# Kernel optimization log

Hardware: AMD Instinct MI355X
Metric: run time of the kernel (lower is better)

The kernel has to match this reference:

```python
import jax, jax.numpy as jnp
import numpy as np

NUM_HEADS = 16
ROPE_BASE = 10000.0


def _rope(x):
    """Standard rotary embedding. x: (B, H, T, Dh), positions 0..T-1."""
    T, Dh = x.shape[-2], x.shape[-1]
    half = Dh // 2
    inv_freq = 1.0 / (ROPE_BASE ** (jnp.arange(half, dtype=jnp.float32) / half))
    ang = jnp.arange(T, dtype=jnp.float32)[:, None] * inv_freq[None, :]  # (T, half)
    cos, sin = jnp.cos(ang), jnp.sin(ang)
    x1, x2 = x[..., :half], x[..., half:]
    return jnp.concatenate([x1 * cos - x2 * sin, x1 * sin + x2 * cos], axis=-1)


def setup_inputs() -> dict:
    key = jax.random.key(0)
    ks = jax.random.split(key, 5)
    B, N, D = 8, 1025, 1024
    s = 1.0 / np.sqrt(D)
    return {
        "x": jax.random.normal(ks[0], (B, N, D), jnp.float32),
        "wq": jax.random.normal(ks[1], (D, D), jnp.float32) * s,
        "wk": jax.random.normal(ks[2], (D, D), jnp.float32) * s,
        "wv": jax.random.normal(ks[3], (D, D), jnp.float32) * s,
        "q_bias": jnp.zeros((D,), jnp.float32),
        "v_bias": jnp.zeros((D,), jnp.float32),
        "w_out": jax.random.normal(ks[4], (D, D), jnp.float32) * s,
        "b_out": jnp.zeros((D,), jnp.float32),
    }


def reference(x, wq, wk, wv, q_bias, v_bias, w_out, b_out):
    B, N, D = x.shape
    H = NUM_HEADS
    Dh = D // H
    scale = Dh ** -0.5

    q = x @ wq + q_bias           # (B, N, D)
    k = x @ wk
    v = x @ wv + v_bias

    def split_heads(t):  # (B, N, D) -> (B, H, N, Dh)
        return t.reshape(B, N, H, Dh).transpose(0, 2, 1, 3)

    q, k, v = split_heads(q), split_heads(k), split_heads(v)

    # RoPE on all tokens except the first (CLS)
    q = jnp.concatenate([q[:, :, :1, :], _rope(q[:, :, 1:, :])], axis=2)
    k = jnp.concatenate([k[:, :, :1, :], _rope(k[:, :, 1:, :])], axis=2)

    attn = jnp.einsum('bhqd,bhkd->bhqk', q * scale, k)
    attn = jax.nn.softmax(attn, axis=-1)
    out = jnp.einsum('bhqk,bhkd->bhqd', attn, v)  # (B, H, N, Dh)
    out = out.transpose(0, 2, 1, 3).reshape(B, N, D)
    return out @ w_out + b_out
```

## Files before the change

kernel.cpp:

```cpp
#include <hip/hip_runtime.h>

typedef unsigned short u16;
typedef __attribute__((ext_vector_type(8))) short  short8;
typedef __attribute__((ext_vector_type(8))) __bf16 bf16x8;
typedef __attribute__((ext_vector_type(4))) float  f32x4;

#define DEV __device__ __forceinline__

#define BATCH 8
#define SEQ   1025
#define DMODEL 1024
#define NHEAD 16
#define DH    64
#define MROWS (BATCH*SEQ)
#define VPAD  1152
#define KROWS 1088

DEV float bf2f(u16 u) { union { unsigned int i; float f; } v; v.i = ((unsigned int)u) << 16; return v.f; }
DEV u16 f2bf(float f) {
  union { float f; unsigned int i; } v; v.f = f;
  unsigned int x = v.i;
  return (u16)((x + 0x7fffu + ((x >> 16) & 1u)) >> 16);
}

DEV f32x4 mfma16(bf16x8 a, bf16x8 b, f32x4 c) {
  return __builtin_amdgcn_mfma_f32_16x16x32_bf16(a, b, c, 0, 0, 0);
}

DEV void gload_lds16(const void* g, void* s) {
  __builtin_amdgcn_global_load_lds(
      (const __attribute__((address_space(1))) void*)g,
      (__attribute__((address_space(3))) void*)s, 16, 0, 0);
}

DEV float exp2_fast(float x) { float r; asm("v_exp_f32 %0, %1" : "=v"(r) : "v"(x)); return r; }
DEV unsigned cvt_pk_bf16(float lo, float hi) {
  unsigned r;
  asm("v_cvt_pk_bf16_f32 %0, %1, %2" : "=v"(r) : "v"(lo), "v"(hi));
  return r;
}


__global__ void cast_x_kernel(const float* __restrict__ in, u16* __restrict__ out, int n8) {
  int i = blockIdx.x * blockDim.x + threadIdx.x;
  if (i >= n8) return;
  const float4* p = (const float4*)in + (size_t)i * 2;
  float4 a = p[0], b = p[1];
  short8 o;
  o[0] = (short)f2bf(a.x); o[1] = (short)f2bf(a.y); o[2] = (short)f2bf(a.z); o[3] = (short)f2bf(a.w);
  o[4] = (short)f2bf(b.x); o[5] = (short)f2bf(b.y); o[6] = (short)f2bf(b.z); o[7] = (short)f2bf(b.w);
  *(short8*)(out + (size_t)i * 8) = o;
}

__global__ void wt_transpose(const float* __restrict__ wq, const float* __restrict__ wk,
                             const float* __restrict__ wv, const float* __restrict__ wo,
                             u16* __restrict__ wtqkv, u16* __restrict__ wtout) {
  __shared__ float tile[64][65];
  int z = blockIdx.z;
  const float* src = (z == 0) ? wq : (z == 1) ? wk : (z == 2) ? wv : wo;
  int k0 = blockIdx.x * 64, n0 = blockIdx.y * 64;
  int c = threadIdx.x & 63, rq = threadIdx.x >> 6;
#pragma unroll
  for (int p = 0; p < 16; ++p) {
    int r = p * 4 + rq;
    tile[r][c] = src[(size_t)(k0 + r) * 1024 + n0 + c];
  }
  __syncthreads();
  u16* dst = (z < 3) ? (wtqkv + (size_t)z * 1024 * 1024) : wtout;
#pragma unroll
  for (int p = 0; p < 16; ++p) {
    int r = p * 4 + rq;
    dst[(size_t)(n0 + r) * 1024 + k0 + c] = f2bf(tile[c][r]);
  }
}

__global__ void rope_table_kernel(float* __restrict__ cost, float* __restrict__ sint) {
  int i = blockIdx.x * blockDim.x + threadIdx.x;
  if (i >= 1024 * 32) return;
  int pos = i >> 5, d = i & 31;
  float inv = powf(10000.0f, -(float)d / 32.0f);
  float ang = (float)pos * inv;
  cost[i] = cosf(ang);
  sint[i] = sinf(ang);
}

template <int F32OUT>
__global__ __launch_bounds__(256) void gemm128(const u16* __restrict__ A,
    const u16* __restrict__ Bw, void* __restrict__ Cout,
    const float* __restrict__ bias, int Mrows, int ldC) {
  __shared__ char smem[32768];
  const int t = threadIdx.x;
  const int wid = t >> 6, lane = t & 63;
  const int l4 = lane >> 4, l15 = lane & 15;
  const int wr = wid >> 1, wc = wid & 1;
  const long rowA0 = (long)blockIdx.x * 128;
  const long rowB0 = (long)blockIdx.y * 128;

  f32x4 acc[4][4];
#pragma unroll
  for (int m = 0; m < 4; ++m)
#pragma unroll
    for (int n = 0; n < 4; ++n) { f32x4 z = {0.f,0.f,0.f,0.f}; acc[m][n] = z; }

  const int srow = t >> 3;
  const int scol = (t & 7) * 8;

  for (int k0 = 0; k0 < 1024; k0 += 64) {
    __syncthreads();
#pragma unroll
    for (int i = 0; i < 4; ++i) {
      const u16* ga = A  + (rowA0 + i * 32 + srow) * 1024 + k0 + scol;
      gload_lds16(ga, smem + i * 4096 + wid * 1024);
      const u16* gb = Bw + (rowB0 + i * 32 + srow) * 1024 + k0 + scol;
      gload_lds16(gb, smem + 16384 + i * 4096 + wid * 1024);
    }
    __syncthreads();

    bf16x8 af[4][2], bfr[4][2];
#pragma unroll
    for (int m = 0; m < 4; ++m)
#pragma unroll
      for (int kk = 0; kk < 2; ++kk)
        af[m][kk] = *(const bf16x8*)(smem + (wr * 64 + m * 16 + l15) * 128 + kk * 64 + l4 * 16);
#pragma unroll
    for (int n = 0; n < 4; ++n)
#pragma unroll
      for (int kk = 0; kk < 2; ++kk)
        bfr[n][kk] = *(const bf16x8*)(smem + 16384 + (wc * 64 + n * 16 + l15) * 128 + kk * 64 + l4 * 16);

#pragma unroll
    for (int m = 0; m < 4; ++m)
#pragma unroll
      for (int n = 0; n < 4; ++n)
#pragma unroll
        for (int kk = 0; kk < 2; ++kk)
          acc[m][n] = mfma16(af[m][kk], bfr[n][kk], acc[m][n]);
  }

#pragma unroll
  for (int m = 0; m < 4; ++m)
#pragma unroll
    for (int rg = 0; rg < 4; ++rg) {
      long row = rowA0 + wr * 64 + m * 16 + l4 * 4 + rg;
      if (row >= Mrows) continue;
#pragma unroll
      for (int n = 0; n < 4; ++n) {
        long col = rowB0 + wc * 64 + n * 16 + l15;
        float val = acc[m][n][rg];
        if (F32OUT) ((float*)Cout)[row * ldC + col] = val + bias[col];
        else        ((u16*) Cout)[row * ldC + col] = f2bf(val);
      }
    }
}

#define QSCALE (0.125f * 1.44269504088896341f)
__global__ void rope_qk(const u16* __restrict__ cq, const float* __restrict__ qb,
                        const float* __restrict__ cost, const float* __restrict__ sint,
                        u16* __restrict__ Qh, u16* __restrict__ Kh) {
  int idx = blockIdx.x * 256 + threadIdx.x;
  if (idx >= MROWS * NHEAD) return;
  int h = idx & 15, row = idx >> 4;
  int b = row / SEQ, n = row - b * SEQ;
  const u16* src = cq + (size_t)row * 3072 + h * 64;
  size_t dq = ((size_t)(b * 16 + h) * SEQ   + n) * 64;
  size_t dk = ((size_t)(b * 16 + h) * KROWS + n) * 64;
  bool dorope = (n > 0);
  const float* ct = cost + (size_t)(n - 1) * 32;
  const float* st = sint + (size_t)(n - 1) * 32;
#pragma unroll
  for (int i = 0; i < 4; ++i) {
    short8 qlo = *(const short8*)(src + i * 8);
    short8 qhi = *(const short8*)(src + 32 + i * 8);
    short8 klo = *(const short8*)(src + 1024 + i * 8);
    short8 khi = *(const short8*)(src + 1024 + 32 + i * 8);
    short8 oqlo, oqhi, oklo, okhi;
#pragma unroll
    for (int j = 0; j < 8; ++j) {
      int d = i * 8 + j;
      float q1 = bf2f((u16)qlo[j]) + qb[h * 64 + d];
      float q2 = bf2f((u16)qhi[j]) + qb[h * 64 + 32 + d];
      float k1 = bf2f((u16)klo[j]);
      float k2 = bf2f((u16)khi[j]);
      float c = dorope ? ct[d] : 1.0f;
      float s = dorope ? st[d] : 0.0f;
      oqlo[j] = (short)f2bf((q1 * c - q2 * s) * QSCALE);
      oqhi[j] = (short)f2bf((q1 * s + q2 * c) * QSCALE);
      oklo[j] = (short)f2bf(k1 * c - k2 * s);
      okhi[j] = (short)f2bf(k1 * s + k2 * c);
    }
    *(short8*)(Qh + dq + i * 8)      = oqlo;
    *(short8*)(Qh + dq + 32 + i * 8) = oqhi;
    *(short8*)(Kh + dk + i * 8)      = oklo;
    *(short8*)(Kh + dk + 32 + i * 8) = okhi;
  }
}

__global__ void v_transpose(const u16* __restrict__ cq, const float* __restrict__ vb,
                            u16* __restrict__ VTh) {
  __shared__ float tile[64][65];
  int bh = blockIdx.y, b = bh >> 4, h = bh & 15;
  int n0 = blockIdx.x * 64;
  int c = threadIdx.x & 63, rq = threadIdx.x >> 6;
#pragma unroll
  for (int p = 0; p < 16; ++p) {
    int r = p * 4 + rq;
    int n = n0 + r;
    float v = 0.f;
    if (n < SEQ) v = bf2f(cq[(size_t)(b * SEQ + n) * 3072 + 2048 + h * 64 + c]) + vb[h * 64 + c];
    tile[r][c] = v;
  }
  __syncthreads();
#pragma unroll
  for (int p = 0; p < 16; ++p) {
    int d = p * 4 + rq;
    VTh[((size_t)bh * 64 + d) * VPAD + n0 + c] = f2bf(tile[c][d]);
  }
}

DEV void stage_rows(const u16* __restrict__ g, size_t strideElems, char* lbase,
                    int wid, int lane) {
#pragma unroll
  for (int s = 0; s < 2; ++s) {
    int off = s * 4096 + wid * 1024 + lane * 16;
    int r = off >> 7, cs = (off >> 4) & 7;
    const u16* src = g + (size_t)r * strideElems + ((cs ^ (r & 7)) << 3);
    gload_lds16(src, lbase + s * 4096 + wid * 1024);
  }
}

__global__ __launch_bounds__(256, 4) void attn128(const u16* __restrict__ Qh,
    const u16* __restrict__ Kh, const u16* __restrict__ VTh,
    u16* __restrict__ xattn) {
  __shared__ char lds[32768];
  const int wg = blockIdx.x;
  const int x = (wg & 7) * 144 + (wg >> 3);
  const int qt = x % 9, bh = x / 9;
  const int b = bh >> 4, h = bh & 15;
  const int t = threadIdx.x, w = t >> 6, lane = t & 63;
  const int l4 = lane >> 4, l15 = lane & 15;
  const u16* Qb = Qh + (size_t)bh * (SEQ * 64);
  const u16* Kb = Kh + (size_t)bh * (KROWS * 64);
  const u16* Vb = VTh + (size_t)bh * (64 * VPAD);
  const int q0 = qt * 128 + w * 32;
  const int srcb = l15 + ((l4 & 1) << 5);
  const bool hi4 = (l4 >> 1) != 0;

  bf16x8 aq[2][2];
#pragma unroll
  for (int m = 0; m < 2; ++m) {
    int qr = q0 + m * 16 + l15; if (qr > SEQ - 1) qr = SEQ - 1;
    aq[m][0] = *(const bf16x8*)(Qb + (size_t)qr * 64 + l4 * 8);
    aq[m][1] = *(const bf16x8*)(Qb + (size_t)qr * 64 + 32 + l4 * 8);
  }
  bf16x8 ones;
  { union { unsigned u[4]; bf16x8 v; } ou;
    ou.u[0] = ou.u[1] = ou.u[2] = ou.u[3] = 0x3F803F80u; ones = ou.v; }

  f32x4 o[2][4], osum[2];
  float mrow[2];
#pragma unroll
  for (int m = 0; m < 2; ++m) {
#pragma unroll
    for (int n = 0; n < 4; ++n) { f32x4 z = {0.f,0.f,0.f,0.f}; o[m][n] = z; }
    f32x4 z = {0.f,0.f,0.f,0.f}; osum[m] = z;
    mrow[m] = -1e30f;
  }

  stage_rows(Kb, 64, lds, w, lane);
  stage_rows(Vb, VPAD, lds + 16384, w, lane);
  asm volatile("s_waitcnt vmcnt(0)" ::: "memory");
  __syncthreads();

  int cur = 0;
  for (int kt = 0; kt < 17; ++kt) {
    const int kb = kt * 64;
    if (kt < 16) {
      stage_rows(Kb + (size_t)(kb + 64) * 64, 64, lds + (cur ^ 1) * 8192, w, lane);
      stage_rows(Vb + (kb + 64), VPAD, lds + 16384 + (cur ^ 1) * 8192, w, lane);
    }
    const char* Kl = lds + cur * 8192;
    const char* Vl = lds + 16384 + cur * 8192;

    f32x4 s[2][4];
#pragma unroll
    for (int tt = 0; tt < 4; ++tt) {
      const int kr = tt * 16 + l15;
      const char* kp = Kl + kr * 128;
      bf16x8 bk0 = *(const bf16x8*)(kp + ((l4       ^ (kr & 7)) << 4));
      bf16x8 bk1 = *(const bf16x8*)(kp + (((4 + l4) ^ (kr & 7)) << 4));
#pragma unroll
      for (int m = 0; m < 2; ++m) {
        f32x4 z = {0.f,0.f,0.f,0.f};
        z = mfma16(bk0, aq[m][0], z);
        z = mfma16(bk1, aq[m][1], z);
        s[m][tt] = z;
      }
    }

    if (kt == 16) {
#pragma unroll
      for (int m = 0; m < 2; ++m) {
        s[m][0][0] = (l4 == 0) ? s[m][0][0] : -1e30f;
        s[m][0][1] = -1e30f; s[m][0][2] = -1e30f; s[m][0][3] = -1e30f;
#pragma unroll
        for (int tt = 1; tt < 4; ++tt) {
          s[m][tt][0] = -1e30f; s[m][tt][1] = -1e30f; s[m][tt][2] = -1e30f; s[m][tt][3] = -1e30f;
        }
      }
    }

    float tmax[2];
#pragma unroll
    for (int m = 0; m < 2; ++m) {
      float a0 = fmaxf(fmaxf(s[m][0][0], s[m][0][1]), fmaxf(s[m][0][2], s[m][0][3]));
      float a1 = fmaxf(fmaxf(s[m][1][0], s[m][1][1]), fmaxf(s[m][1][2], s[m][1][3]));
      float a2 = fmaxf(fmaxf(s[m][2][0], s[m][2][1]), fmaxf(s[m][2][2], s[m][2][3]));
      float a3 = fmaxf(fmaxf(s[m][3][0], s[m][3][1]), fmaxf(s[m][3][2], s[m][3][3]));
      float tm = fmaxf(fmaxf(a0, a1), fmaxf(a2, a3));
      tm = fmaxf(tm, __shfl_xor(tm, 16));
      tm = fmaxf(tm, __shfl_xor(tm, 32));
      tmax[m] = tm;
    }

    int needR = (tmax[0] > mrow[0] + 8.0f) || (tmax[1] > mrow[1] + 8.0f);
    if (__any(needR)) {
#pragma unroll
      for (int m = 0; m < 2; ++m) {
        float mnew = fmaxf(mrow[m], tmax[m]);
        float alpha = exp2_fast(mrow[m] - mnew);
        mrow[m] = mnew;
        float al[4];
#pragma unroll
        for (int rg = 0; rg < 4; ++rg) al[rg] = __shfl(alpha, l4 * 4 + rg);
#pragma unroll
        for (int n = 0; n < 4; ++n)
#pragma unroll
          for (int rg = 0; rg < 4; ++rg) o[m][n][rg] *= al[rg];
#pragma unroll
        for (int rg = 0; rg < 4; ++rg) osum[m][rg] *= al[rg];
      }
    }

    unsigned pk[2][4][2];
#pragma unroll
    for (int m = 0; m < 2; ++m)
#pragma unroll
      for (int tt = 0; tt < 4; ++tt) {
        float p0 = exp2_fast(s[m][tt][0] - mrow[m]);
        float p1 = exp2_fast(s[m][tt][1] - mrow[m]);
        float p2 = exp2_fast(s[m][tt][2] - mrow[m]);
        float p3 = exp2_fast(s[m][tt][3] - mrow[m]);
        pk[m][tt][0] = cvt_pk_bf16(p0, p1);
        pk[m][tt][1] = cvt_pk_bf16(p2, p3);
      }

#pragma unroll
    for (int kk = 0; kk < 2; ++kk) {
      bf16x8 pa[2];
#pragma unroll
      for (int m = 0; m < 2; ++m) {
        union { unsigned u[4]; bf16x8 v; } pu;
#pragma unroll
        for (int bb = 0; bb < 2; ++bb)
#pragma unroll
          for (int pr = 0; pr < 2; ++pr) {
            unsigned t0 = (unsigned)__shfl((int)pk[m][2 * kk][pr],     srcb + bb * 16);
            unsigned t1 = (unsigned)__shfl((int)pk[m][2 * kk + 1][pr], srcb + bb * 16);
            pu.u[bb * 2 + pr] = hi4 ? t1 : t0;
          }
        pa[m] = pu.v;
      }
#pragma unroll
      for (int n = 0; n < 4; ++n) {
        const int vr = n * 16 + l15;
        bf16x8 bv = *(const bf16x8*)(Vl + vr * 128 + (((kk * 4 + l4) ^ (vr & 7)) << 4));
#pragma unroll
        for (int m = 0; m < 2; ++m)
          o[m][n] = mfma16(pa[m], bv, o[m][n]);
      }
#pragma unroll
      for (int m = 0; m < 2; ++m)
        osum[m] = mfma16(pa[m], ones, osum[m]);
    }

    asm volatile("s_waitcnt vmcnt(0)" ::: "memory");
    __syncthreads();
    cur ^= 1;
  }

#pragma unroll
  for (int m = 0; m < 2; ++m)
#pragma unroll
    for (int n = 0; n < 4; ++n)
#pragma unroll
      for (int rg = 0; rg < 4; ++rg) {
        int qrow = q0 + m * 16 + l4 * 4 + rg;
        if (qrow < SEQ)
          xattn[(size_t)(b * SEQ + qrow) * 1024 + h * 64 + n * 16 + l15] =
              f2bf(o[m][n][rg] / osum[m][rg]);
      }
}


extern "C" void kernel_launch(void* const* d_in, const int* in_sizes, int n_in,
                              void* d_out, int out_size, void* d_ws, size_t ws_size,
                              hipStream_t stream) {
  const float* x      = (const float*)d_in[0];
  const float* wq     = (const float*)d_in[1];
  const float* wk     = (const float*)d_in[2];
  const float* wv     = (const float*)d_in[3];
  const float* q_bias = (const float*)d_in[4];
  const float* v_bias = (const float*)d_in[5];
  const float* w_out  = (const float*)d_in[6];
  const float* b_out  = (const float*)d_in[7];

  char* ws = (char*)d_ws;
  size_t off = 0;
  auto alc = [&](size_t bytes) { size_t r = off; off += (bytes + 255) & ~(size_t)255; return r; };

  u16*  x_bf  = (u16*)(ws + alc((size_t)MROWS * 1024 * 2));
  u16*  wtqkv = (u16*)(ws + alc((size_t)3072 * 1024 * 2));
  u16*  wtout = (u16*)(ws + alc((size_t)1024 * 1024 * 2));
  u16*  xattn = (u16*)(ws + alc((size_t)MROWS * 1024 * 2));
  u16*  cqkv  = (u16*)(ws + alc((size_t)MROWS * 3072 * 2));
  u16*  Qhp   = (u16*)(ws + alc((size_t)128 * SEQ * 64 * 2));
  u16*  Khp   = (u16*)(ws + alc((size_t)128 * KROWS * 64 * 2));
  u16*  VThp  = (u16*)(ws + alc((size_t)128 * 64 * VPAD * 2));
  float* cost = (float*)(ws + alc((size_t)1024 * 32 * 4));
  float* sint = (float*)(ws + alc((size_t)1024 * 32 * 4));
  (void)ws_size; (void)in_sizes; (void)n_in; (void)out_size;

  cast_x_kernel<<<4100, 256, 0, stream>>>(x, x_bf, MROWS * 1024 / 8);
  wt_transpose<<<dim3(16, 16, 4), 256, 0, stream>>>(wq, wk, wv, w_out, wtqkv, wtout);
  rope_table_kernel<<<128, 256, 0, stream>>>(cost, sint);
  gemm128<0><<<dim3(65, 24), 256, 0, stream>>>(x_bf, wtqkv, (void*)cqkv, nullptr, MROWS, 3072);
  rope_qk<<<513, 256, 0, stream>>>(cqkv, q_bias, cost, sint, Qhp, Khp);
  v_transpose<<<dim3(18, 128), 256, 0, stream>>>(cqkv, v_bias, VThp);
  attn128<<<dim3(1152), 256, 0, stream>>>(Qhp, Khp, VThp, xattn);
  gemm128<1><<<dim3(65, 8), 256, 0, stream>>>(xattn, wtout, d_out, b_out, MROWS, 1024);
}
```

Baseline: 294.7 us.

## Fuse RoPE, bias and V transpose into QKV GEMM epilogue; remap tiles for L2

The QKV projection GEMM now applies the q bias, RoPE and Q scaling directly in its epilogue. It also writes Q/K in head-major layout and transposes V through LDS into the padded VT buffer. This removes the intermediate cqkv buffer and two separate kernels, along with their global-memory round trips and launches. Both GEMMs switch to a 1-D grid with a grouped, XCD-aware tile mapping to improve L2 reuse. The trade-off is scattered 2-byte epilogue stores instead of vectorized writes, plus extra epilogue work in the GEMM.

```diff
diff --git a/kernel.cpp b/kernel.cpp
--- a/kernel.cpp
+++ b/kernel.cpp
@@ -38,6 +38,12 @@
   unsigned r;
   asm("v_cvt_pk_bf16_f32 %0, %1, %2" : "=v"(r) : "v"(lo), "v"(hi));
   return r;
+}
+
+DEV void map_tiles(int f, int MT, int NT, int& mt, int& nt) {
+  int body = (MT & ~7) * NT;
+  if (f >= body) { int r = f - body; mt = (MT & ~7) + r / NT; nt = r % NT; }
+  else { int sr = f / (8 * NT); int rem = f - sr * 8 * NT; nt = rem >> 3; mt = sr * 8 + (rem & 7); }
 }
 
 
@@ -84,17 +90,21 @@
   sint[i] = sinf(ang);
 }
 
-template <int F32OUT>
-__global__ __launch_bounds__(256) void gemm128(const u16* __restrict__ A,
-    const u16* __restrict__ Bw, void* __restrict__ Cout,
-    const float* __restrict__ bias, int Mrows, int ldC) {
+#define QSCALE (0.125f * 1.44269504088896341f)
+
+__global__ __launch_bounds__(256) void gemm_qkv(const u16* __restrict__ A,
+    const u16* __restrict__ Bw, const float* __restrict__ qb, const float* __restrict__ vb,
+    const float* __restrict__ ct, const float* __restrict__ st,
+    u16* __restrict__ Qh, u16* __restrict__ Kh, u16* __restrict__ VTh) {
   __shared__ char smem[32768];
+  int mt, nt;
+  { int wg = blockIdx.x; int f = (wg & 7) * 195 + (wg >> 3); map_tiles(f, 65, 24, mt, nt); }
   const int t = threadIdx.x;
   const int wid = t >> 6, lane = t & 63;
   const int l4 = lane >> 4, l15 = lane & 15;
   const int wr = wid >> 1, wc = wid & 1;
-  const long rowA0 = (long)blockIdx.x * 128;
-  const long rowB0 = (long)blockIdx.y * 128;
+  const long rowA0 = (long)mt * 128;
+  const long rowB0 = (long)nt * 128;
 
   f32x4 acc[4][4];
 #pragma unroll
@@ -137,84 +147,139 @@
           acc[m][n] = mfma16(af[m][kk], bfr[n][kk], acc[m][n]);
   }
 
+  const int sel = nt >> 3;
+  const int h = (nt & 7) * 2 + wc;
+
+  if (sel < 2) {
+#pragma unroll
+    for (int m = 0; m < 4; ++m)
+#pragma unroll
+      for (int rg = 0; rg < 4; ++rg) {
+        long row = rowA0 + wr * 64 + m * 16 + l4 * 4 + rg;
+        if (row >= MROWS) continue;
+        int b = (int)(row / SEQ), nl = (int)(row - (long)b * SEQ);
+        bool dorope = nl > 0;
+        const float* ctp = ct + (size_t)(nl - 1) * 32;
+        const float* stp = st + (size_t)(nl - 1) * 32;
+#pragma unroll
+        for (int n = 0; n < 2; ++n) {
+          int d = n * 16 + l15;
+          float c = dorope ? ctp[d] : 1.0f;
+          float s_ = dorope ? stp[d] : 0.0f;
+          float v1 = acc[m][n][rg], v2 = acc[m][n + 2][rg];
+          if (sel == 0) { v1 += qb[h * 64 + d]; v2 += qb[h * 64 + 32 + d]; }
+          float o1 = v1 * c - v2 * s_;
+          float o2 = v1 * s_ + v2 * c;
+          if (sel == 0) {
+            size_t base = ((size_t)(b * 16 + h) * SEQ + nl) * 64 + d;
+            Qh[base]      = f2bf(o1 * QSCALE);
+            Qh[base + 32] = f2bf(o2 * QSCALE);
+          } else {
+            size_t base = ((size_t)(b * 16 + h) * KROWS + nl) * 64 + d;
+            Kh[base]      = f2bf(o1);
+            Kh[base + 32] = f2bf(o2);
+          }
+        }
+      }
+  } else {
+    __syncthreads();
+#pragma unroll
+    for (int m = 0; m < 4; ++m)
+#pragma unroll
+      for (int n = 0; n < 4; ++n) {
+        int co = wc * 64 + n * 16 + l15;
+        int d = n * 16 + l15;
+        float bv = vb[h * 64 + d];
+#pragma unroll
+        for (int rg = 0; rg < 4; ++rg) {
+          int ro = wr * 64 + m * 16 + l4 * 4 + rg;
+          *(u16*)(smem + co * 256 + ((ro * 2) ^ ((co & 7) << 4))) = f2bf(acc[m][n][rg] + bv);
+        }
+      }
+    __syncthreads();
+    const int c = t & 127, half = t >> 7;
+    const int hh = (nt & 7) * 2 + (c >> 6);
+    const int d = c & 63;
+#pragma unroll
+    for (int j = 0; j < 8; ++j) {
+      int t0 = half * 64 + j * 8;
+      short8 v8 = *(const short8*)(smem + c * 256 + ((t0 * 2) ^ ((c & 7) << 4)));
+#pragma unroll
+      for (int e = 0; e < 8; ++e) {
+        long r = rowA0 + t0 + e;
+        if (r >= MROWS) continue;
+        int b = (int)(r / SEQ), nl = (int)(r - (long)b * SEQ);
+        VTh[((size_t)(b * 16 + hh) * 64 + d) * VPAD + nl] = (u16)v8[e];
+      }
+    }
+  }
+}
+
+__global__ __launch_bounds__(256) void gemm_out(const u16* __restrict__ A,
+    const u16* __restrict__ Bw, float* __restrict__ Cout, const float* __restrict__ bias) {
+  __shared__ char smem[32768];
+  int mt, nt;
+  { int wg = blockIdx.x; int f = (wg & 7) * 65 + (wg >> 3); map_tiles(f, 65, 8, mt, nt); }
+  const int t = threadIdx.x;
+  const int wid = t >> 6, lane = t & 63;
+  const int l4 = lane >> 4, l15 = lane & 15;
+  const int wr = wid >> 1, wc = wid & 1;
+  const long rowA0 = (long)mt * 128;
+  const long rowB0 = (long)nt * 128;
+
+  f32x4 acc[4][4];
+#pragma unroll
+  for (int m = 0; m < 4; ++m)
+#pragma unroll
+    for (int n = 0; n < 4; ++n) { f32x4 z = {0.f,0.f,0.f,0.f}; acc[m][n] = z; }
+
+  const int srow = t >> 3;
+  const int scol = (t & 7) * 8;
+
+  for (int k0 = 0; k0 < 1024; k0 += 64) {
+    __syncthreads();
+#pragma unroll
+    for (int i = 0; i < 4; ++i) {
+      const u16* ga = A  + (rowA0 + i * 32 + srow) * 1024 + k0 + scol;
+      gload_lds16(ga, smem + i * 4096 + wid * 1024);
+      const u16* gb = Bw + (rowB0 + i * 32 + srow) * 1024 + k0 + scol;
+      gload_lds16(gb, smem + 16384 + i * 4096 + wid * 1024);
+    }
+    __syncthreads();
+
+    bf16x8 af[4][2], bfr[4][2];
+#pragma unroll
+    for (int m = 0; m < 4; ++m)
+#pragma unroll
+      for (int kk = 0; kk < 2; ++kk)
+        af[m][kk] = *(const bf16x8*)(smem + (wr * 64 + m * 16 + l15) * 128 + kk * 64 + l4 * 16);
+#pragma unroll
+    for (int n = 0; n < 4; ++n)
+#pragma unroll
+      for (int kk = 0; kk < 2; ++kk)
+        bfr[n][kk] = *(const bf16x8*)(smem + 16384 + (wc * 64 + n * 16 + l15) * 128 + kk * 64 + l4 * 16);
+
+#pragma unroll
+    for (int m = 0; m < 4; ++m)
+#pragma unroll
+      for (int n = 0; n < 4; ++n)
+#pragma unroll
+        for (int kk = 0; kk < 2; ++kk)
+          acc[m][n] = mfma16(af[m][kk], bfr[n][kk], acc[m][n]);
+  }
+
 #pragma unroll
   for (int m = 0; m < 4; ++m)
 #pragma unroll
     for (int rg = 0; rg < 4; ++rg) {
       long row = rowA0 + wr * 64 + m * 16 + l4 * 4 + rg;
-      if (row >= Mrows) continue;
+      if (row >= MROWS) continue;
 #pragma unroll
       for (int n = 0; n < 4; ++n) {
         long col = rowB0 + wc * 64 + n * 16 + l15;
-        float val = acc[m][n][rg];
-        if (F32OUT) ((float*)Cout)[row * ldC + col] = val + bias[col];
-        else        ((u16*) Cout)[row * ldC + col] = f2bf(val);
-      }
-    }
-}
-
-#define QSCALE (0.125f * 1.44269504088896341f)
-__global__ void rope_qk(const u16* __restrict__ cq, const float* __restrict__ qb,
-                        const float* __restrict__ cost, const float* __restrict__ sint,
-                        u16* __restrict__ Qh, u16* __restrict__ Kh) {
-  int idx = blockIdx.x * 256 + threadIdx.x;
-  if (idx >= MROWS * NHEAD) return;
-  int h = idx & 15, row = idx >> 4;
-  int b = row / SEQ, n = row - b * SEQ;
-  const u16* src = cq + (size_t)row * 3072 + h * 64;
-  size_t dq = ((size_t)(b * 16 + h) * SEQ   + n) * 64;
-  size_t dk = ((size_t)(b * 16 + h) * KROWS + n) * 64;
-  bool dorope = (n > 0);
-  const float* ct = cost + (size_t)(n - 1) * 32;
-  const float* st = sint + (size_t)(n - 1) * 32;
-#pragma unroll
-  for (int i = 0; i < 4; ++i) {
-    short8 qlo = *(const short8*)(src + i * 8);
-    short8 qhi = *(const short8*)(src + 32 + i * 8);
-    short8 klo = *(const short8*)(src + 1024 + i * 8);
-    short8 khi = *(const short8*)(src + 1024 + 32 + i * 8);
-    short8 oqlo, oqhi, oklo, okhi;
-#pragma unroll
-    for (int j = 0; j < 8; ++j) {
-      int d = i * 8 + j;
-      float q1 = bf2f((u16)qlo[j]) + qb[h * 64 + d];
-      float q2 = bf2f((u16)qhi[j]) + qb[h * 64 + 32 + d];
-      float k1 = bf2f((u16)klo[j]);
-      float k2 = bf2f((u16)khi[j]);
-      float c = dorope ? ct[d] : 1.0f;
-      float s = dorope ? st[d] : 0.0f;
-      oqlo[j] = (short)f2bf((q1 * c - q2 * s) * QSCALE);
-      oqhi[j] = (short)f2bf((q1 * s + q2 * c) * QSCALE);
-      oklo[j] = (short)f2bf(k1 * c - k2 * s);
-      okhi[j] = (short)f2bf(k1 * s + k2 * c);
-    }
-    *(short8*)(Qh + dq + i * 8)      = oqlo;
-    *(short8*)(Qh + dq + 32 + i * 8) = oqhi;
-    *(short8*)(Kh + dk + i * 8)      = oklo;
-    *(short8*)(Kh + dk + 32 + i * 8) = okhi;
-  }
-}
-
-__global__ void v_transpose(const u16* __restrict__ cq, const float* __restrict__ vb,
-                            u16* __restrict__ VTh) {
-  __shared__ float tile[64][65];
-  int bh = blockIdx.y, b = bh >> 4, h = bh & 15;
-  int n0 = blockIdx.x * 64;
-  int c = threadIdx.x & 63, rq = threadIdx.x >> 6;
-#pragma unroll
-  for (int p = 0; p < 16; ++p) {
-    int r = p * 4 + rq;
-    int n = n0 + r;
-    float v = 0.f;
-    if (n < SEQ) v = bf2f(cq[(size_t)(b * SEQ + n) * 3072 + 2048 + h * 64 + c]) + vb[h * 64 + c];
-    tile[r][c] = v;
-  }
-  __syncthreads();
-#pragma unroll
-  for (int p = 0; p < 16; ++p) {
-    int d = p * 4 + rq;
-    VTh[((size_t)bh * 64 + d) * VPAD + n0 + c] = f2bf(tile[c][d]);
-  }
+        Cout[row * 1024 + col] = acc[m][n][rg] + bias[col];
+      }
+    }
 }
 
 DEV void stage_rows(const u16* __restrict__ g, size_t strideElems, char* lbase,
@@ -422,7 +487,6 @@
   u16*  wtqkv = (u16*)(ws + alc((size_t)3072 * 1024 * 2));
   u16*  wtout = (u16*)(ws + alc((size_t)1024 * 1024 * 2));
   u16*  xattn = (u16*)(ws + alc((size_t)MROWS * 1024 * 2));
-  u16*  cqkv  = (u16*)(ws + alc((size_t)MROWS * 3072 * 2));
   u16*  Qhp   = (u16*)(ws + alc((size_t)128 * SEQ * 64 * 2));
   u16*  Khp   = (u16*)(ws + alc((size_t)128 * KROWS * 64 * 2));
   u16*  VThp  = (u16*)(ws + alc((size_t)128 * 64 * VPAD * 2));
@@ -433,9 +497,8 @@
   cast_x_kernel<<<4100, 256, 0, stream>>>(x, x_bf, MROWS * 1024 / 8);
   wt_transpose<<<dim3(16, 16, 4), 256, 0, stream>>>(wq, wk, wv, w_out, wtqkv, wtout);
   rope_table_kernel<<<128, 256, 0, stream>>>(cost, sint);
-  gemm128<0><<<dim3(65, 24), 256, 0, stream>>>(x_bf, wtqkv, (void*)cqkv, nullptr, MROWS, 3072);
-  rope_qk<<<513, 256, 0, stream>>>(cqkv, q_bias, cost, sint, Qhp, Khp);
-  v_transpose<<<dim3(18, 128), 256, 0, stream>>>(cqkv, v_bias, VThp);
+  gemm_qkv<<<dim3(1560), 256, 0, stream>>>(x_bf, wtqkv, q_bias, v_bias, cost, sint,
+                                           Qhp, Khp, VThp);
   attn128<<<dim3(1152), 256, 0, stream>>>(Qhp, Khp, VThp, xattn);
-  gemm128<1><<<dim3(65, 8), 256, 0, stream>>>(xattn, wtout, d_out, b_out, MROWS, 1024);
-}
+  gemm_out<<<dim3(520), 256, 0, stream>>>(xattn, wtout, (float*)d_out, b_out);
+}
```

Result: slower. 305.6 us (+3.7%).

## Replace QKV GEMM with 256x256 double-buffered swizzled LDS kernel and XCD-aware tile mapping

Applied to the files above, without the earlier changes.

The QKV projection now uses a 512-thread kernel with 256x256 output tiles. It double-buffers LDS, prefetching the next K slice while computing the current one. The LDS layout is XOR-swizzled to avoid bank conflicts, and MFMA issue priority is raised. Block indices are remapped so each XCD works on neighbouring tiles for L2 reuse, and the output GEMM gets a similar XCD-grouped tile mapping. The aim is higher arithmetic intensity and hidden load latency. In exchange the kernel uses 128KB of LDS and many accumulator registers, and the last M tile reads past the valid rows into padded workspace.

```diff
diff --git a/kernel.cpp b/kernel.cpp
--- a/kernel.cpp
+++ b/kernel.cpp
@@ -84,17 +84,123 @@
   sint[i] = sinf(ang);
 }
 
-template <int F32OUT>
-__global__ __launch_bounds__(256) void gemm128(const u16* __restrict__ A,
-    const u16* __restrict__ Bw, void* __restrict__ Cout,
-    const float* __restrict__ bias, int Mrows, int ldC) {
+#define QSCALE (0.125f * 1.44269504088896341f)
+
+DEV void stage_issue(const u16* __restrict__ gtile, char* dst, int wid, int lane, int s) {
+  int tt = wid * 64 + lane;
+  int row = s * 64 + (tt >> 3);
+  int cs = (((tt & 7) ^ (row & 7)) << 3);
+  gload_lds16(gtile + (size_t)row * 1024 + cs, dst + s * 8192 + wid * 1024);
+}
+
+__global__ __launch_bounds__(512, 2) void gemm256(const u16* __restrict__ A,
+    const u16* __restrict__ Bw, u16* __restrict__ Cout) {
+  __shared__ char lds[131072];
+  int mt, nt;
+  {
+    int orig = blockIdx.x;
+    int xcd = orig & 7;
+    int f = (xcd < 4 ? xcd * 50 : 200 + (xcd - 4) * 49) + (orig >> 3);
+    if (f < 384) { int sr = f / 48, rem = f % 48; nt = rem >> 2; mt = sr * 4 + (rem & 3); }
+    else { mt = 32; nt = f - 384; }
+  }
+  const int t = threadIdx.x;
+  const int wid = t >> 6, lane = t & 63;
+  const int l4 = lane >> 4, l15 = lane & 15;
+  const int wrow = wid >> 2, wcol = wid & 3;
+  const long rowA0 = (long)mt * 256;
+  const long rowB0 = (long)nt * 256;
+
+  f32x4 acc[8][4];
+#pragma unroll
+  for (int m = 0; m < 8; ++m)
+#pragma unroll
+    for (int n = 0; n < 4; ++n) { f32x4 z = {0.f,0.f,0.f,0.f}; acc[m][n] = z; }
+
+#pragma unroll
+  for (int s = 0; s < 4; ++s) stage_issue(A  + rowA0 * 1024, lds,         wid, lane, s);
+#pragma unroll
+  for (int s = 0; s < 4; ++s) stage_issue(Bw + rowB0 * 1024, lds + 65536, wid, lane, s);
+  asm volatile("s_waitcnt vmcnt(0)" ::: "memory");
+  __syncthreads();
+
+  int cur = 0;
+  for (int kt = 0; kt < 16; ++kt) {
+    const char* Al = lds + cur * 32768;
+    const char* Bl = lds + 65536 + cur * 32768;
+    char* An = lds + (cur ^ 1) * 32768;
+    char* Bn = lds + 65536 + (cur ^ 1) * 32768;
+    const u16* gA = A  + rowA0 * 1024 + (kt + 1) * 64;
+    const u16* gB = Bw + rowB0 * 1024 + (kt + 1) * 64;
+    const bool pf = kt < 15;
+
+#pragma unroll
+    for (int kk = 0; kk < 2; ++kk) {
+      bf16x8 bfr[4];
+#pragma unroll
+      for (int n = 0; n < 4; ++n) {
+        int r = wcol * 64 + n * 16 + l15;
+        bfr[n] = *(const bf16x8*)(Bl + r * 128 + ((kk * 64 + l4 * 16) ^ ((r & 7) << 4)));
+      }
+#pragma unroll
+      for (int mh = 0; mh < 2; ++mh) {
+        if (pf) {
+          if (kk == 0 && mh == 0) { stage_issue(gA, An, wid, lane, 0); stage_issue(gA, An, wid, lane, 1); }
+          if (kk == 0 && mh == 1) { stage_issue(gA, An, wid, lane, 2); stage_issue(gA, An, wid, lane, 3); }
+          if (kk == 1 && mh == 0) { stage_issue(gB, Bn, wid, lane, 0); stage_issue(gB, Bn, wid, lane, 1); }
+          if (kk == 1 && mh == 1) { stage_issue(gB, Bn, wid, lane, 2); stage_issue(gB, Bn, wid, lane, 3); }
+        }
+        bf16x8 af[4];
+#pragma unroll
+        for (int m = 0; m < 4; ++m) {
+          int r = wrow * 128 + (mh * 4 + m) * 16 + l15;
+          af[m] = *(const bf16x8*)(Al + r * 128 + ((kk * 64 + l4 * 16) ^ ((r & 7) << 4)));
+        }
+        __builtin_amdgcn_s_setprio(1);
+#pragma unroll
+        for (int m = 0; m < 4; ++m)
+#pragma unroll
+          for (int n = 0; n < 4; ++n)
+            acc[mh * 4 + m][n] = mfma16(af[m], bfr[n], acc[mh * 4 + m][n]);
+        __builtin_amdgcn_s_setprio(0);
+      }
+    }
+    asm volatile("s_waitcnt vmcnt(0)" ::: "memory");
+    __syncthreads();
+    cur ^= 1;
+  }
+
+#pragma unroll
+  for (int m = 0; m < 8; ++m)
+#pragma unroll
+    for (int rg = 0; rg < 4; ++rg) {
+      long row = rowA0 + wrow * 128 + m * 16 + l4 * 4 + rg;
+      if (row >= MROWS) continue;
+#pragma unroll
+      for (int n = 0; n < 4; ++n) {
+        long col = rowB0 + wcol * 64 + n * 16 + l15;
+        Cout[row * 3072 + col] = f2bf(acc[m][n][rg]);
+      }
+    }
+}
+
+DEV void map_tiles(int f, int MT, int NT, int& mt, int& nt) {
+  int body = (MT & ~7) * NT;
+  if (f >= body) { int r = f - body; mt = (MT & ~7) + r / NT; nt = r % NT; }
+  else { int sr = f / (8 * NT); int rem = f - sr * 8 * NT; nt = rem >> 3; mt = sr * 8 + (rem & 7); }
+}
+
+__global__ __launch_bounds__(256) void gemm_out(const u16* __restrict__ A,
+    const u16* __restrict__ Bw, float* __restrict__ Cout, const float* __restrict__ bias) {
   __shared__ char smem[32768];
+  int mt, nt;
+  { int wg = blockIdx.x; int f = (wg & 7) * 65 + (wg >> 3); map_tiles(f, 65, 8, mt, nt); }
   const int t = threadIdx.x;
   const int wid = t >> 6, lane = t & 63;
   const int l4 = lane >> 4, l15 = lane & 15;
   const int wr = wid >> 1, wc = wid & 1;
-  const long rowA0 = (long)blockIdx.x * 128;
-  const long rowB0 = (long)blockIdx.y * 128;
+  const long rowA0 = (long)mt * 128;
+  const long rowB0 = (long)nt * 128;
 
   f32x4 acc[4][4];
 #pragma unroll
@@ -142,18 +248,15 @@
 #pragma unroll
     for (int rg = 0; rg < 4; ++rg) {
       long row = rowA0 + wr * 64 + m * 16 + l4 * 4 + rg;
-      if (row >= Mrows) continue;
+      if (row >= MROWS) continue;
 #pragma unroll
       for (int n = 0; n < 4; ++n) {
         long col = rowB0 + wc * 64 + n * 16 + l15;
-        float val = acc[m][n][rg];
-        if (F32OUT) ((float*)Cout)[row * ldC + col] = val + bias[col];
-        else        ((u16*) Cout)[row * ldC + col] = f2bf(val);
-      }
-    }
-}
-
-#define QSCALE (0.125f * 1.44269504088896341f)
+        Cout[row * 1024 + col] = acc[m][n][rg] + bias[col];
+      }
+    }
+}
+
 __global__ void rope_qk(const u16* __restrict__ cq, const float* __restrict__ qb,
                         const float* __restrict__ cost, const float* __restrict__ sint,
                         u16* __restrict__ Qh, u16* __restrict__ Kh) {
@@ -422,7 +525,7 @@
   u16*  wtqkv = (u16*)(ws + alc((size_t)3072 * 1024 * 2));
   u16*  wtout = (u16*)(ws + alc((size_t)1024 * 1024 * 2));
   u16*  xattn = (u16*)(ws + alc((size_t)MROWS * 1024 * 2));
-  u16*  cqkv  = (u16*)(ws + alc((size_t)MROWS * 3072 * 2));
+  u16*  cqkv  = (u16*)(ws + alc((size_t)8448 * 3072 * 2));
   u16*  Qhp   = (u16*)(ws + alc((size_t)128 * SEQ * 64 * 2));
   u16*  Khp   = (u16*)(ws + alc((size_t)128 * KROWS * 64 * 2));
   u16*  VThp  = (u16*)(ws + alc((size_t)128 * 64 * VPAD * 2));
@@ -433,9 +536,9 @@
   cast_x_kernel<<<4100, 256, 0, stream>>>(x, x_bf, MROWS * 1024 / 8);
   wt_transpose<<<dim3(16, 16, 4), 256, 0, stream>>>(wq, wk, wv, w_out, wtqkv, wtout);
   rope_table_kernel<<<128, 256, 0, stream>>>(cost, sint);
-  gemm128<0><<<dim3(65, 24), 256, 0, stream>>>(x_bf, wtqkv, (void*)cqkv, nullptr, MROWS, 3072);
+  gemm256<<<dim3(396), 512, 0, stream>>>(x_bf, wtqkv, cqkv);
   rope_qk<<<513, 256, 0, stream>>>(cqkv, q_bias, cost, sint, Qhp, Khp);
   v_transpose<<<dim3(18, 128), 256, 0, stream>>>(cqkv, v_bias, VThp);
   attn128<<<dim3(1152), 256, 0, stream>>>(Qhp, Khp, VThp, xattn);
-  gemm128<1><<<dim3(65, 8), 256, 0, stream>>>(xattn, wtout, d_out, b_out, MROWS, 1024);
-}
+  gemm_out<<<dim3(520), 256, 0, stream>>>(xattn, wtout, (float*)d_out, b_out);
+}
```

After: 259.1 us. 1.14x faster.
